# Optimization experiments

Measured on AMD Instinct MI355X. Metric: run time of the kernel, lower is better.

## Reference

```python
import jax, jax.numpy as jnp
import numpy as np

N = 50000          # num nodes
E = 600000         # num edges
F_IN = 128         # num_features
H = 128            # graph_hidden_dim
R = 2              # num_relations
L = 3              # n_layers_conv
BN_EPS = 1e-5
BN_BETA = 1e-4     # BatchNorm bias init per module code


def setup_inputs() -> dict:
    key = jax.random.key(0)
    ks = jax.random.split(key, 9)
    s_in = 1.0 / np.sqrt(F_IN)
    s_h = 1.0 / np.sqrt(H)
    return {
        "x": jax.random.normal(ks[0], (N, F_IN), jnp.float32),
        "edge_index": jax.random.randint(ks[1], (2, E), 0, N, jnp.int32),
        "edge_type": jax.random.randint(ks[2], (E,), 0, R, jnp.int32),
        "W0_rel": jax.random.normal(ks[3], (R, F_IN, H), jnp.float32) * s_in,
        "W0_root": jax.random.normal(ks[4], (F_IN, H), jnp.float32) * s_in,
        "b0": jnp.zeros((H,), jnp.float32),
        "Ws_rel": jax.random.normal(ks[5], (L, R, H, H), jnp.float32) * s_h,
        "Ws_root": jax.random.normal(ks[6], (L, H, H), jnp.float32) * s_h,
        "bs": jnp.zeros((L, H), jnp.float32),
    }


def batchnorm(x):
    # training-mode BatchNorm1d over nodes; weight=1, bias=1e-4 (per init)
    mu = jnp.mean(x, axis=0)
    var = jnp.mean((x - mu) ** 2, axis=0)  # biased var, as torch uses for norm
    return (x - mu) * jax.lax.rsqrt(var + BN_EPS) + BN_BETA


def rgcn_conv(x, src, dst, edge_type, W_rel, W_root, b):
    # PyG RGCNConv, aggr='mean': per-relation mean of x[src] at dst,
    # then per-relation linear, plus root transform and bias.
    seg = dst * R + edge_type  # combined (node, relation) segment id
    msgs = x[src]                                   # [E, d] gather
    sums = jax.ops.segment_sum(msgs, seg, num_segments=N * R)
    cnts = jax.ops.segment_sum(jnp.ones((src.shape[0],), x.dtype), seg,
                               num_segments=N * R)
    mean = sums.reshape(N, R, -1) / jnp.maximum(cnts, 1.0).reshape(N, R, 1)
    out = jnp.einsum('nrd,rdh->nh', mean, W_rel) + x @ W_root + b
    return out


def reference(x, edge_index, edge_type, W0_rel, W0_root, b0, Ws_rel, Ws_root, bs):
    src, dst = edge_index[0], edge_index[1]
    h = batchnorm(x)
    h = jax.nn.relu(rgcn_conv(h, src, dst, edge_type, W0_rel, W0_root, b0))
    for i in range(L):
        h_ = batchnorm(h)
        h_ = jax.nn.relu(rgcn_conv(h_, src, dst, edge_type,
                                   Ws_rel[i], Ws_root[i], bs[i]))
        h = h + h_  # conv_residual=True
    return h  # gconv_dropout == 0
```

## Files before the change

### kernel.cpp

```cpp
#include <hip/hip_runtime.h>
#include <hip/hip_bf16.h>

#define N_NODES 50000
#define N_EDGES 600000
#define F 128
#define R 2
#define NLAYER 4
#define NSEG (N_NODES * R)
#define SEGP (NSEG / 8)
#define NSCB 98
#define NB 384
#define STATS_STRIDE 2048
#define AGGB 6250
#define BN_EPS 1e-5f
#define BETA 1e-4f

typedef __hip_bfloat16 bf16;
typedef __attribute__((ext_vector_type(8))) short short8;
typedef __attribute__((ext_vector_type(4))) short short4x;
typedef __attribute__((ext_vector_type(4))) float floatx4;

__device__ __forceinline__ float b2f(short s) {
    union { unsigned u; float f; } c;
    c.u = ((unsigned)(unsigned short)s) << 16;
    return c.f;
}

__global__ void k_wt(const float* __restrict__ W0_rel, const float* __restrict__ W0_root,
                     const float* __restrict__ Ws_rel, const float* __restrict__ Ws_root,
                     bf16* __restrict__ Bt) {
    int idx = blockIdx.x * 256 + threadIdx.x;
    if (idx >= NLAYER * NB * F) return;
    int l = idx / (NB * F);
    int rem = idx % (NB * F);
    int j = rem / F, d = rem % F;
    float v;
    if (j < 256) {
        int r = j >> 7, c = j & 127;
        v = (l == 0) ? W0_rel[(r * F + d) * F + c]
                     : Ws_rel[((size_t)((l - 1) * R + r) * F + d) * F + c];
    } else {
        int c = j - 256;
        v = (l == 0) ? W0_root[d * F + c]
                     : Ws_root[((size_t)(l - 1) * F + d) * F + c];
    }
    Bt[idx] = __float2bfloat16(v);
}

__global__ void k_seg(const int* __restrict__ dst, const int* __restrict__ et,
                      int* __restrict__ seg) {
    int e = blockIdx.x * 256 + threadIdx.x;
    if (e < N_EDGES) seg[e] = dst[e] * R + et[e];
}

__global__ void k_count(const int* __restrict__ seg, int* __restrict__ cnt) {
    int g = blockIdx.x & 7;
    int lo = g * SEGP, hi = lo + SEGP;
    for (int e = (blockIdx.x >> 3) * 256 + threadIdx.x; e < N_EDGES; e += 65536) {
        int s = seg[e];
        if (s >= lo && s < hi) atomicAdd(&cnt[s], 1);
    }
}

__global__ void k_scan1(const int* __restrict__ cnt, int* __restrict__ off,
                        int* __restrict__ bsum) {
    int t = threadIdx.x;
    int g = blockIdx.x * 1024 + t;
    int v = (g < NSEG) ? cnt[g] : 0;
    int lane = t & 63;
    int wv = t >> 6;
    int x = v;
    for (int d = 1; d < 64; d <<= 1) {
        int y = __shfl_up(x, d, 64);
        if (lane >= d) x += y;
    }
    __shared__ int wtot[16];
    if (lane == 63) wtot[wv] = x;
    __syncthreads();
    if (t < 16) {
        int s = wtot[t];
        for (int d = 1; d < 16; d <<= 1) {
            int y = __shfl_up(s, d, 64);
            if (t >= d) s += y;
        }
        wtot[t] = s;
    }
    __syncthreads();
    int wpre = (wv == 0) ? 0 : wtot[wv - 1];
    int incl = x + wpre;
    if (g < NSEG) off[g] = incl - v;
    if (t == 1023) bsum[blockIdx.x] = incl;
}

__global__ void k_scan2(int* __restrict__ bsum) {
    __shared__ int s[128];
    int t = threadIdx.x;
    int v = (t < NSCB) ? bsum[t] : 0;
    s[t] = v;
    __syncthreads();
    for (int d = 1; d < 128; d <<= 1) {
        int y = (t >= d) ? s[t - d] : 0;
        __syncthreads();
        s[t] += y;
        __syncthreads();
    }
    if (t < NSCB) bsum[t] = s[t] - v;
}

__global__ void k_scan3(int* __restrict__ off, const int* __restrict__ bsum) {
    int g = blockIdx.x * 1024 + threadIdx.x;
    if (g < NSEG) off[g] += bsum[blockIdx.x];
}

__global__ void k_fill(const int* __restrict__ src, const int* __restrict__ seg,
                       const int* __restrict__ off,
                       int* __restrict__ fill, int* __restrict__ esrc) {
    int g = blockIdx.x & 7;
    int lo = g * SEGP, hi = lo + SEGP;
    for (int e = (blockIdx.x >> 3) * 256 + threadIdx.x; e < N_EDGES; e += 65536) {
        int s = seg[e];
        if (s >= lo && s < hi) {
            int idx = off[s] + atomicAdd(&fill[s], 1);
            esrc[idx] = src[e];
        }
    }
}

__global__ void k_bnstats(const float* __restrict__ h, float* __restrict__ gs) {
    int c = threadIdx.x & 127;
    int rl = threadIdx.x >> 7;
    float s = 0.f, q = 0.f;
    for (int r = blockIdx.x * 2 + rl; r < N_NODES; r += gridDim.x * 2) {
        float v = h[(size_t)r * F + c];
        s += v; q += v * v;
    }
    __shared__ float ls[256], lq[256];
    ls[threadIdx.x] = s; lq[threadIdx.x] = q;
    __syncthreads();
    if (rl == 0) {
        atomicAdd(&gs[c], ls[c] + ls[c + 128]);
        atomicAdd(&gs[128 + c], lq[c] + lq[c + 128]);
    }
}

__launch_bounds__(512)
__global__ void k_gemm(const void* __restrict__ hin, int in_bf16,
                       const float* __restrict__ gs,
                       const bf16* __restrict__ Bt, const float* __restrict__ bias,
                       bf16* __restrict__ y, bf16* __restrict__ z) {
    __shared__ bf16 As[64 * 136];
    __shared__ bf16 Bs[128 * 136];
    int t = threadIdx.x;
    int m0 = blockIdx.x * 64;
    int c4 = (t & 31) * 4;
    float mu[4], rs[4];
    for (int c = 0; c < 4; c++) {
        float ssum = 0.f, qsum = 0.f;
        #pragma unroll
        for (int k = 0; k < 8; k++) {
            ssum += gs[k * 256 + c4 + c];
            qsum += gs[k * 256 + 128 + c4 + c];
        }
        float mm = ssum * (1.0f / N_NODES);
        float qq = qsum * (1.0f / N_NODES);
        mu[c] = mm;
        rs[c] = rsqrtf(qq - mm * mm + BN_EPS);
    }
    int r0 = t >> 5;
    for (int it = 0; it < 4; it++) {
        int row = r0 + it * 16;
        int m = m0 + row;
        float f0 = 0.f, f1 = 0.f, f2 = 0.f, f3 = 0.f;
        if (m < N_NODES) {
            if (in_bf16) {
                short4x v = *(const short4x*)((const bf16*)hin + (size_t)m * F + c4);
                f0 = b2f(v.x); f1 = b2f(v.y); f2 = b2f(v.z); f3 = b2f(v.w);
            } else {
                float4 v = *(const float4*)((const float*)hin + (size_t)m * F + c4);
                f0 = v.x; f1 = v.y; f2 = v.z; f3 = v.w;
            }
        }
        bf16 o[4];
        o[0] = __float2bfloat16((f0 - mu[0]) * rs[0] + BETA);
        o[1] = __float2bfloat16((f1 - mu[1]) * rs[1] + BETA);
        o[2] = __float2bfloat16((f2 - mu[2]) * rs[2] + BETA);
        o[3] = __float2bfloat16((f3 - mu[3]) * rs[3] + BETA);
        *(double*)(As + row * 136 + c4) = *(const double*)o;
    }
    __syncthreads();
    int w = t >> 6;
    int lane = t & 63;
    int msub = w & 3;
    int nh = w >> 2;
    int lm = lane & 15;
    int lq = lane >> 4;
    short8 a[4];
    for (int ki = 0; ki < 4; ki++)
        a[ki] = *(const short8*)(As + (msub * 16 + lm) * 136 + ki * 32 + lq * 8);
    int m = m0 + msub * 16 + lm;
    for (int ci = 0; ci < 3; ci++) {
        __syncthreads();
        {
            const bf16* bsrc = Bt + (size_t)ci * 128 * F;
            for (int rr = 0; rr < 4; rr++) {
                int idx = rr * 512 + t;
                int row = idx >> 4;
                int kc = idx & 15;
                short8 v = *(const short8*)(bsrc + row * F + kc * 8);
                *(short8*)(Bs + row * 136 + kc * 8) = v;
            }
        }
        __syncthreads();
        for (int tt = 0; tt < 4; tt++) {
            int nt = nh * 4 + tt;
            short8 b[4];
            for (int ki = 0; ki < 4; ki++)
                b[ki] = *(const short8*)(Bs + (nt * 16 + lm) * 136 + ki * 32 + lq * 8);
            floatx4 acc = {0.f, 0.f, 0.f, 0.f};
            for (int ki = 0; ki < 4; ki++)
                acc = __builtin_amdgcn_mfma_f32_16x16x32_bf16(b[ki], a[ki], acc, 0, 0, 0);
            int n0 = ci * 128 + nt * 16 + lq * 4;
            if (m < N_NODES) {
                if (ci < 2) {
                    union { bf16 o[4]; double d; } u;
                    u.o[0] = __float2bfloat16(acc[0]);
                    u.o[1] = __float2bfloat16(acc[1]);
                    u.o[2] = __float2bfloat16(acc[2]);
                    u.o[3] = __float2bfloat16(acc[3]);
                    *(double*)(y + (size_t)m * 256 + n0) = u.d;
                } else {
                    float4 bv = *(const float4*)(bias + (n0 - 256));
                    union { bf16 o[4]; double d; } u;
                    u.o[0] = __float2bfloat16(acc[0] + bv.x);
                    u.o[1] = __float2bfloat16(acc[1] + bv.y);
                    u.o[2] = __float2bfloat16(acc[2] + bv.z);
                    u.o[3] = __float2bfloat16(acc[3] + bv.w);
                    *(double*)(z + (size_t)m * F + (n0 - 256)) = u.d;
                }
            }
        }
    }
}

__launch_bounds__(512)
__global__ void k_aggregate(const bf16* __restrict__ y, const bf16* __restrict__ z,
                            const int* __restrict__ cnt, const int* __restrict__ off,
                            const int* __restrict__ esrc,
                            const bf16* __restrict__ hres, bf16* __restrict__ hb_out,
                            float* __restrict__ out_f32,
                            float* __restrict__ gs_next, int layer) {
    int wid = (blockIdx.x * 512 + threadIdx.x) >> 6;
    int lane = threadIdx.x & 63;
    int n = wid;
    int half = lane >> 5;
    int hl = lane & 31;
    int c4 = hl * 4;
    int2 cc = *(const int2*)(cnt + n * R);
    int o0 = off[n * R];
    int myc = half ? cc.y : cc.x;
    int myo = half ? (o0 + cc.x) : o0;
    float myinv = (myc > 0) ? 1.0f / (float)myc : 0.f;
    const bf16* yb = y + half * 128 + c4;
    float s0 = 0.f, s1 = 0.f, s2 = 0.f, s3 = 0.f;
    for (int i = 0; i < myc; i += 8) {
        int sn[8];
        #pragma unroll
        for (int k = 0; k < 8; k++) {
            int valid = (i + k < myc);
            sn[k] = esrc[valid ? (myo + i + k) : myo];
        }
        short4x p[8];
        #pragma unroll
        for (int k = 0; k < 8; k++)
            p[k] = *(const short4x*)(yb + (size_t)sn[k] * 256);
        #pragma unroll
        for (int k = 0; k < 8; k++) {
            float wk = (i + k < myc) ? myinv : 0.f;
            s0 = fmaf(b2f(p[k].x), wk, s0);
            s1 = fmaf(b2f(p[k].y), wk, s1);
            s2 = fmaf(b2f(p[k].z), wk, s2);
            s3 = fmaf(b2f(p[k].w), wk, s3);
        }
    }
    float t0 = __shfl_xor(s0, 32, 64);
    float t1 = __shfl_xor(s1, 32, 64);
    float t2 = __shfl_xor(s2, 32, 64);
    float t3 = __shfl_xor(s3, 32, 64);
    __shared__ float ls[8][128], lq[8][128];
    int wv = threadIdx.x >> 6;
    if (half == 0) {
        short4x zb = *(const short4x*)(z + (size_t)n * F + c4);
        float4 hp = {0.f, 0.f, 0.f, 0.f};
        if (layer > 0) {
            short4x hv = *(const short4x*)(hres + (size_t)n * F + c4);
            hp.x = b2f(hv.x); hp.y = b2f(hv.y); hp.z = b2f(hv.z); hp.w = b2f(hv.w);
        }
        float4 o4;
        o4.x = fmaxf(b2f(zb.x) + s0 + t0, 0.f) + hp.x;
        o4.y = fmaxf(b2f(zb.y) + s1 + t1, 0.f) + hp.y;
        o4.z = fmaxf(b2f(zb.z) + s2 + t2, 0.f) + hp.z;
        o4.w = fmaxf(b2f(zb.w) + s3 + t3, 0.f) + hp.w;
        if (out_f32) {
            *(float4*)(out_f32 + (size_t)n * F + c4) = o4;
        } else {
            short4x st;
            st.x = *(short*)&(((bf16*)&st)[0]);
            bf16 ob[4];
            ob[0] = __float2bfloat16(o4.x);
            ob[1] = __float2bfloat16(o4.y);
            ob[2] = __float2bfloat16(o4.z);
            ob[3] = __float2bfloat16(o4.w);
            *(double*)(hb_out + (size_t)n * F + c4) = *(const double*)ob;
            if (gs_next) {
                float r0v = b2f(*(const short*)&ob[0]);
                float r1v = b2f(*(const short*)&ob[1]);
                float r2v = b2f(*(const short*)&ob[2]);
                float r3v = b2f(*(const short*)&ob[3]);
                ls[wv][c4 + 0] = r0v; ls[wv][c4 + 1] = r1v;
                ls[wv][c4 + 2] = r2v; ls[wv][c4 + 3] = r3v;
                lq[wv][c4 + 0] = r0v * r0v; lq[wv][c4 + 1] = r1v * r1v;
                lq[wv][c4 + 2] = r2v * r2v; lq[wv][c4 + 3] = r3v * r3v;
            }
        }
    }
    if (gs_next) {
        __syncthreads();
        int t = threadIdx.x;
        float* gsc = gs_next + (blockIdx.x & 7) * 256;
        if (t < 128) {
            float S = ((ls[0][t] + ls[1][t]) + (ls[2][t] + ls[3][t]))
                    + ((ls[4][t] + ls[5][t]) + (ls[6][t] + ls[7][t]));
            atomicAdd(&gsc[t], S);
        } else if (t < 256) {
            int c = t - 128;
            float Q = ((lq[0][c] + lq[1][c]) + (lq[2][c] + lq[3][c]))
                    + ((lq[4][c] + lq[5][c]) + (lq[6][c] + lq[7][c]));
            atomicAdd(&gsc[128 + c], Q);
        }
    }
}

extern "C" void kernel_launch(void* const* d_in, const int* in_sizes, int n_in,
                              void* d_out, int out_size, void* d_ws, size_t ws_size,
                              hipStream_t stream) {
    const float* x       = (const float*)d_in[0];
    const int*   eidx    = (const int*)d_in[1];
    const int*   etype   = (const int*)d_in[2];
    const float* W0_rel  = (const float*)d_in[3];
    const float* W0_root = (const float*)d_in[4];
    const float* b0      = (const float*)d_in[5];
    const float* Ws_rel  = (const float*)d_in[6];
    const float* Ws_root = (const float*)d_in[7];
    const float* bs      = (const float*)d_in[8];
    const int* src = eidx;
    const int* dst = eidx + N_EDGES;

    char* w = (char*)d_ws;
    bf16*  hb  = (bf16*)w;  w += (size_t)N_NODES * F * 2;
    bf16*  z   = (bf16*)w;  w += (size_t)N_NODES * F * 2;
    bf16*  y   = (bf16*)w;  w += (size_t)N_NODES * 256 * 2;
    bf16*  Bt  = (bf16*)w;  w += (size_t)NLAYER * NB * F * 2;
    int* cnt   = (int*)w;   w += (size_t)NSEG * 4;
    int* fill  = (int*)w;   w += (size_t)NSEG * 4;
    float* stats = (float*)w; w += (size_t)NLAYER * STATS_STRIDE * 4;
    int* off   = (int*)w;   w += (size_t)NSEG * 4;
    int* esrc  = (int*)w;   w += (size_t)N_EDGES * 4;
    int* segb  = (int*)w;   w += (size_t)N_EDGES * 4;
    int* bsum  = (int*)w;   w += 128 * 4;

    hipMemsetAsync(cnt, 0, (size_t)NSEG * 4 * 2 + (size_t)NLAYER * STATS_STRIDE * 4, stream);
    k_wt<<<(NLAYER * NB * F + 255) / 256, 256, 0, stream>>>(W0_rel, W0_root, Ws_rel, Ws_root, Bt);
    k_seg<<<(N_EDGES + 255) / 256, 256, 0, stream>>>(dst, etype, segb);
    k_count<<<2048, 256, 0, stream>>>(segb, cnt);
    k_scan1<<<NSCB, 1024, 0, stream>>>(cnt, off, bsum);
    k_scan2<<<1, 128, 0, stream>>>(bsum);
    k_scan3<<<NSCB, 1024, 0, stream>>>(off, bsum);
    k_fill<<<2048, 256, 0, stream>>>(src, segb, off, fill, esrc);
    k_bnstats<<<512, 256, 0, stream>>>(x, stats);

    for (int l = 0; l < NLAYER; l++) {
        const float* gsl = stats + (size_t)l * STATS_STRIDE;
        const float* bias = (l == 0) ? b0 : (bs + (size_t)(l - 1) * F);
        const void* hin = (l == 0) ? (const void*)x : (const void*)hb;
        k_gemm<<<(N_NODES + 63) / 64, 512, 0, stream>>>(
            hin, (l > 0) ? 1 : 0, gsl, Bt + (size_t)l * NB * F, bias, y, z);
        k_aggregate<<<AGGB, 512, 0, stream>>>(
            y, z, cnt, off, esrc, hb, hb,
            (l == 3) ? (float*)d_out : nullptr,
            (l < 3) ? (float*)(stats + (size_t)(l + 1) * STATS_STRIDE) : nullptr, l);
    }
}
```

Measured before the change: 423.7 us.

## Drop scan2 launch, read GEMM weights directly, widen aggregation gather batch

Measured after the change: 552.7 us. 30.5% more time.

```diff
diff --git a/kernel.cpp b/kernel.cpp
--- a/kernel.cpp
+++ b/kernel.cpp
@@ -92,24 +92,16 @@
     if (t == 1023) bsum[blockIdx.x] = incl;
 }
 
-__global__ void k_scan2(int* __restrict__ bsum) {
-    __shared__ int s[128];
-    int t = threadIdx.x;
-    int v = (t < NSCB) ? bsum[t] : 0;
-    s[t] = v;
-    __syncthreads();
-    for (int d = 1; d < 128; d <<= 1) {
-        int y = (t >= d) ? s[t - d] : 0;
-        __syncthreads();
-        s[t] += y;
-        __syncthreads();
-    }
-    if (t < NSCB) bsum[t] = s[t] - v;
-}
-
 __global__ void k_scan3(int* __restrict__ off, const int* __restrict__ bsum) {
+    __shared__ int pre;
+    if (threadIdx.x == 0) {
+        int p = 0;
+        for (int b = 0; b < blockIdx.x; b++) p += bsum[b];
+        pre = p;
+    }
+    __syncthreads();
     int g = blockIdx.x * 1024 + threadIdx.x;
-    if (g < NSEG) off[g] += bsum[blockIdx.x];
+    if (g < NSEG) off[g] += pre;
 }
 
 __global__ void k_fill(const int* __restrict__ src, const int* __restrict__ seg,
@@ -149,7 +141,6 @@
                        const bf16* __restrict__ Bt, const float* __restrict__ bias,
                        bf16* __restrict__ y, bf16* __restrict__ z) {
     __shared__ bf16 As[64 * 136];
-    __shared__ bf16 Bs[128 * 136];
     int t = threadIdx.x;
     int m0 = blockIdx.x * 64;
     int c4 = (t & 31) * 4;
@@ -199,24 +190,15 @@
         a[ki] = *(const short8*)(As + (msub * 16 + lm) * 136 + ki * 32 + lq * 8);
     int m = m0 + msub * 16 + lm;
     for (int ci = 0; ci < 3; ci++) {
-        __syncthreads();
-        {
-            const bf16* bsrc = Bt + (size_t)ci * 128 * F;
-            for (int rr = 0; rr < 4; rr++) {
-                int idx = rr * 512 + t;
-                int row = idx >> 4;
-                int kc = idx & 15;
-                short8 v = *(const short8*)(bsrc + row * F + kc * 8);
-                *(short8*)(Bs + row * 136 + kc * 8) = v;
-            }
-        }
-        __syncthreads();
         for (int tt = 0; tt < 4; tt++) {
             int nt = nh * 4 + tt;
+            const bf16* brow = Bt + (size_t)(ci * 128 + nt * 16 + lm) * F + lq * 8;
             short8 b[4];
+            #pragma unroll
             for (int ki = 0; ki < 4; ki++)
-                b[ki] = *(const short8*)(Bs + (nt * 16 + lm) * 136 + ki * 32 + lq * 8);
+                b[ki] = *(const short8*)(brow + ki * 32);
             floatx4 acc = {0.f, 0.f, 0.f, 0.f};
+            #pragma unroll
             for (int ki = 0; ki < 4; ki++)
                 acc = __builtin_amdgcn_mfma_f32_16x16x32_bf16(b[ki], a[ki], acc, 0, 0, 0);
             int n0 = ci * 128 + nt * 16 + lq * 4;
@@ -262,19 +244,19 @@
     float myinv = (myc > 0) ? 1.0f / (float)myc : 0.f;
     const bf16* yb = y + half * 128 + c4;
     float s0 = 0.f, s1 = 0.f, s2 = 0.f, s3 = 0.f;
-    for (int i = 0; i < myc; i += 8) {
-        int sn[8];
+    for (int i = 0; i < myc; i += 12) {
+        int sn[12];
         #pragma unroll
-        for (int k = 0; k < 8; k++) {
+        for (int k = 0; k < 12; k++) {
             int valid = (i + k < myc);
             sn[k] = esrc[valid ? (myo + i + k) : myo];
         }
-        short4x p[8];
+        short4x p[12];
         #pragma unroll
-        for (int k = 0; k < 8; k++)
+        for (int k = 0; k < 12; k++)
             p[k] = *(const short4x*)(yb + (size_t)sn[k] * 256);
         #pragma unroll
-        for (int k = 0; k < 8; k++) {
+        for (int k = 0; k < 12; k++) {
             float wk = (i + k < myc) ? myinv : 0.f;
             s0 = fmaf(b2f(p[k].x), wk, s0);
             s1 = fmaf(b2f(p[k].y), wk, s1);
@@ -303,8 +285,6 @@
         if (out_f32) {
             *(float4*)(out_f32 + (size_t)n * F + c4) = o4;
         } else {
-            short4x st;
-            st.x = *(short*)&(((bf16*)&st)[0]);
             bf16 ob[4];
             ob[0] = __float2bfloat16(o4.x);
             ob[1] = __float2bfloat16(o4.y);
@@ -373,7 +353,6 @@
     k_seg<<<(N_EDGES + 255) / 256, 256, 0, stream>>>(dst, etype, segb);
     k_count<<<2048, 256, 0, stream>>>(segb, cnt);
     k_scan1<<<NSCB, 1024, 0, stream>>>(cnt, off, bsum);
-    k_scan2<<<1, 128, 0, stream>>>(bsum);
     k_scan3<<<NSCB, 1024, 0, stream>>>(off, bsum);
     k_fill<<<2048, 256, 0, stream>>>(src, segb, off, fill, esrc);
     k_bnstats<<<512, 256, 0, stream>>>(x, stats);
```
